# Optimization experiments

Hardware: AMD Instinct MI355X
Metric: run time of the kernel (lower is better)

The kernel has to match this reference:

```python
import jax, jax.numpy as jnp
import numpy as np

HID = 256   # hidden_dim
P = 16      # pool_size
EPS = 1e-5


def _ln(x, g, b):
    m = x.mean(-1, keepdims=True)
    v = x.var(-1, keepdims=True)
    return (x - m) * jax.lax.rsqrt(v + EPS) * g + b


def setup_inputs() -> dict:
    key = jax.random.key(0)
    ks = jax.random.split(key, 12)
    B, Cf, H, W = 8, 512, 64, 64
    Cg = Cf // 2
    Co = Cf // 2
    s = 0.02
    d = {}
    d['e_f'] = jax.random.normal(ks[0], (B, Cf, H, W), jnp.float32)
    d['e_g'] = jax.random.normal(ks[1], (B, Cg, H, W), jnp.float32)
    d['l_feat'] = jax.random.normal(ks[2], (B, 768, 20), jnp.float32)
    d['l_mask'] = jnp.ones((B, 20, 1), jnp.float32)
    d['ln_f_g'] = jnp.ones((Cf,), jnp.float32)
    d['ln_f_b'] = jnp.zeros((Cf,), jnp.float32)
    d['ln_g_g'] = jnp.ones((Cg,), jnp.float32)
    d['ln_g_b'] = jnp.zeros((Cg,), jnp.float32)
    d['wq'] = jax.random.normal(ks[3], (Cf, HID), jnp.float32) * s
    d['bq'] = jnp.zeros((HID,), jnp.float32)
    d['wk'] = jax.random.normal(ks[4], (Cg, HID), jnp.float32) * s
    d['bk'] = jnp.zeros((HID,), jnp.float32)
    d['wv'] = jax.random.normal(ks[5], (Cg, HID), jnp.float32) * s
    d['bv'] = jnp.zeros((HID,), jnp.float32)
    d['wo'] = jax.random.normal(ks[6], (HID, HID), jnp.float32) * s
    d['bo'] = jnp.zeros((HID,), jnp.float32)
    d['dw_k'] = jax.random.normal(ks[7], (HID, 1, 3, 3), jnp.float32) * s  # depthwise kernel (OIHW, I=1)
    d['efp_w'] = jax.random.normal(ks[8], (HID, Cf), jnp.float32) * s     # 1x1 conv v_channels->hidden
    d['efp_b'] = jnp.zeros((HID,), jnp.float32)
    d['outc_w'] = jax.random.normal(ks[9], (Co, HID), jnp.float32) * s    # 1x1 conv hidden->out
    d['outc_b'] = jnp.zeros((Co,), jnp.float32)
    d['bn_g'] = jnp.ones((Co,), jnp.float32)
    d['bn_b'] = jnp.zeros((Co,), jnp.float32)
    d['bn_m'] = jnp.zeros((Co,), jnp.float32)
    d['bn_v'] = jnp.ones((Co,), jnp.float32)
    return d


def reference(e_f, e_g, l_feat, l_mask, ln_f_g, ln_f_b, ln_g_g, ln_g_b,
              wq, bq, wk, bk, wv, bv, wo, bo, dw_k, efp_w, efp_b,
              outc_w, outc_b, bn_g, bn_b, bn_m, bn_v):
    B, Cf, H, W = e_f.shape
    # Q = w_qi(LN(e_f))                                  (B, HW, HID)
    q = _ln(e_f.transpose(0, 2, 3, 1), ln_f_g, ln_f_b).reshape(B, H * W, Cf) @ wq + bq
    # K/V projections from LN(e_g)
    g = _ln(e_g.transpose(0, 2, 3, 1), ln_g_g, ln_g_b).reshape(B, H * W, -1)
    k = (g @ wk + bk).reshape(B, H, W, HID)
    v = (g @ wv + bv).reshape(B, H, W, HID)
    # 16x16 max/avg pooling -> (B, Hp*Wp, HID)
    k = jnp.max(k.reshape(B, H // P, P, W // P, P, HID), axis=(2, 4)).reshape(B, -1, HID)
    v = jnp.mean(v.reshape(B, H // P, P, W // P, P, HID), axis=(2, 4)).reshape(B, -1, HID)
    # pooled attention
    attn = jax.nn.softmax(jnp.einsum('bqd,bkd->bqk', q, k) * (HID ** -0.5), axis=-1)
    a_i = jnp.einsum('bqk,bkd->bqd', attn, v)  # (B, HW, HID)
    # depthwise 3x3 conv on Q (NCHW)
    q_nchw = q.reshape(B, H, W, HID).transpose(0, 3, 1, 2)
    dw = jax.lax.conv_general_dilated(q_nchw, dw_k, (1, 1), [(1, 1), (1, 1)],
                                      feature_group_count=HID)
    combined = dw + a_i.reshape(B, H, W, HID).transpose(0, 3, 1, 2)
    comb = combined.transpose(0, 2, 3, 1).reshape(B, H * W, HID) @ wo + bo
    comb = comb.reshape(B, H, W, HID).transpose(0, 3, 1, 2)
    # 1x1 proj of e_f, elementwise gate
    efp = jnp.einsum('bchw,oc->bohw', e_f, efp_w) + efp_b[None, :, None, None]
    e_a = efp * comb
    # out: 1x1 conv + BN (inference) + ReLU (dropout inactive in eval)
    out = jnp.einsum('bchw,oc->bohw', e_a, outc_w) + outc_b[None, :, None, None]
    scale = (bn_g * jax.lax.rsqrt(bn_v + EPS))[None, :, None, None]
    out = (out - bn_m[None, :, None, None]) * scale + bn_b[None, :, None, None]
    return jax.nn.relu(out)
```

## Files before the change

### kernel.cpp

```cpp
#include <hip/hip_runtime.h>
#include <math.h>

#define EPS 1e-5f

typedef __attribute__((ext_vector_type(8))) short bf16x8;
typedef __attribute__((ext_vector_type(4))) float f32x4;

__device__ __forceinline__ unsigned short f2bf(float f) {
    unsigned int u = __float_as_uint(f);
    u += 0x7fff + ((u >> 16) & 1);
    return (unsigned short)(u >> 16);
}
__device__ __forceinline__ float bf2f(unsigned short h) {
    return __uint_as_float(((unsigned int)h) << 16);
}
__device__ __forceinline__ float lof(unsigned int u) {
    return __uint_as_float(u << 16);
}
__device__ __forceinline__ float hif(unsigned int u) {
    return __uint_as_float(u & 0xffff0000u);
}
__device__ __forceinline__ void async16(void* lds, const void* g) {
    __builtin_amdgcn_global_load_lds(
        (const __attribute__((address_space(1))) unsigned int*)g,
        (__attribute__((address_space(3))) unsigned int*)lds, 16, 0, 0);
}

__global__ __launch_bounds__(256) void prep_all(
    const float* __restrict__ lnfg, const float* __restrict__ lnfb,
    const float* __restrict__ wq, const float* __restrict__ bq,
    const float* __restrict__ efpw, const float* __restrict__ efpb,
    const float* __restrict__ lngg, const float* __restrict__ lngb,
    const float* __restrict__ wk, const float* __restrict__ bk,
    const float* __restrict__ wv, const float* __restrict__ bv,
    const float* __restrict__ wo, const float* __restrict__ outcw,
    const float* __restrict__ outcb, const float* __restrict__ bng,
    const float* __restrict__ bnb, const float* __restrict__ bnm,
    const float* __restrict__ bnv, const float* __restrict__ dwk,
    unsigned short* __restrict__ Wb1t, unsigned short* __restrict__ Wb2t,
    unsigned short* __restrict__ Wot, unsigned short* __restrict__ Woc,
    float* __restrict__ dwt,
    float* __restrict__ cs1, float* __restrict__ cst1,
    float* __restrict__ cs2, float* __restrict__ cst2,
    float* __restrict__ scv, float* __restrict__ shv)
{
    int idx = blockIdx.x * 256 + threadIdx.x;
    if (idx < 262144) {
        int n = idx >> 9, k = idx & 511;
        float v = (n < 256) ? lnfg[k] * wq[k * 256 + n]
                            : efpw[(size_t)(n - 256) * 512 + k];
        Wb1t[idx] = f2bf(v);
    } else if (idx < 327680) {
        int j = idx - 262144; int n = j >> 8, k = j & 255;
        Wb2t[j] = f2bf(lngg[k] * wk[k * 256 + n]);
    } else if (idx < 393216) {
        int j = idx - 327680; int n = j >> 8, k = j & 255;
        Wot[j] = f2bf(wo[k * 256 + n]);
    } else if (idx < 458752) {
        int j = idx - 393216;
        Woc[j] = f2bf(outcw[j]);
    } else if (idx < 461056) {
        int j = idx - 458752; int tap = j >> 8, ch = j & 255;
        dwt[j] = dwk[ch * 9 + tap];
    } else if (idx < 462336) {
        int j = idx - 461056;
        if (j < 256) {
            int n = j; float cs = 0.f, ct = 0.f;
            for (int k = 0; k < 512; k++) {
                float w = wq[k * 256 + n];
                cs += lnfg[k] * w; ct += lnfb[k] * w;
            }
            cs1[n] = cs; cst1[n] = ct + bq[n];
        } else if (j < 512) {
            cs1[j] = 0.f; cst1[j] = efpb[j - 256];
        } else if (j < 768) {
            int n = j - 512; float cs = 0.f, ct = 0.f;
            for (int k = 0; k < 256; k++) {
                float w = wk[k * 256 + n];
                cs += lngg[k] * w; ct += lngb[k] * w;
            }
            cs2[n] = cs; cst2[n] = ct + bk[n];
        } else if (j < 1024) {
            int n = j - 768; float cs = 0.f, ct = 0.f;
            for (int k = 0; k < 256; k++) {
                float w = wv[k * 256 + n];
                cs += lngg[k] * w; ct += lngb[k] * w;
            }
            cs2[256 + n] = cs; cst2[256 + n] = ct + bv[n];
        } else {
            int n = j - 1024;
            float s = bng[n] * rsqrtf(bnv[n] + EPS);
            scv[n] = s;
            shv[n] = (outcb[n] - bnm[n]) * s + bnb[n];
        }
    }
}

__global__ __launch_bounds__(256) void transpose_fg(
    const float* __restrict__ ef, const float* __restrict__ eg,
    unsigned short* __restrict__ ef_bf, unsigned short* __restrict__ eg_bf,
    float* __restrict__ pf, float* __restrict__ pfq,
    float* __restrict__ pg, float* __restrict__ pgq)
{
    __shared__ float tile[64][65];
    __shared__ float psum[4][64], pss[4][64];
    int id = blockIdx.x;
    const float* src; unsigned short* dst; float* ps; float* pq;
    int C, cblk, b, p0;
    if (id < 4096) {
        src = ef; dst = ef_bf; ps = pf; pq = pfq; C = 512;
        p0 = (id & 63) * 64; cblk = (id >> 6) & 7; b = id >> 9;
    } else {
        id -= 4096;
        src = eg; dst = eg_bf; ps = pg; pq = pgq; C = 256;
        p0 = (id & 63) * 64; cblk = (id >> 6) & 3; b = id >> 8;
    }
    int c0 = cblk * 64;
    const float* s = src + ((size_t)b * C + c0) * 4096 + p0;
    int t = threadIdx.x;
    int lane = t & 63, grp = t >> 6;
#pragma unroll
    for (int i = 0; i < 16; i++) {
        int c = i * 4 + grp;
        tile[c][lane] = s[(size_t)c * 4096 + lane];
    }
    __syncthreads();
    unsigned short* d = dst + ((size_t)(b * 4096 + p0)) * C + c0;
#pragma unroll
    for (int i = 0; i < 16; i++) {
        int p = i * 4 + grp;
        d[(size_t)p * C + lane] = f2bf(tile[lane][p]);
    }
    float sm = 0.f, sq = 0.f;
#pragma unroll
    for (int j = 0; j < 16; j++) {
        float v = tile[grp * 16 + j][lane];
        sm += v; sq += v * v;
    }
    psum[grp][lane] = sm; pss[grp][lane] = sq;
    __syncthreads();
    if (t < 64) {
        float fs = psum[0][t] + psum[1][t] + psum[2][t] + psum[3][t];
        float fq = pss[0][t] + pss[1][t] + pss[2][t] + pss[3][t];
        ps[cblk * 32768 + b * 4096 + p0 + t] = fs;
        pq[cblk * 32768 + b * 4096 + p0 + t] = fq;
    }
}

__global__ __launch_bounds__(256) void ln_finalize(
    const float* __restrict__ pf, const float* __restrict__ pfq,
    const float* __restrict__ pg, const float* __restrict__ pgq,
    float* __restrict__ mf, float* __restrict__ rf,
    float* __restrict__ mg, float* __restrict__ rg)
{
    int gp = blockIdx.x * 256 + threadIdx.x;
    float s = 0.f, q = 0.f;
#pragma unroll
    for (int i = 0; i < 8; i++) { s += pf[i * 32768 + gp]; q += pfq[i * 32768 + gp]; }
    float m = s * (1.f / 512.f);
    float v = q * (1.f / 512.f) - m * m;
    mf[gp] = m; rf[gp] = rsqrtf(v + EPS);
    s = 0.f; q = 0.f;
#pragma unroll
    for (int i = 0; i < 4; i++) { s += pg[i * 32768 + gp]; q += pgq[i * 32768 + gp]; }
    m = s * (1.f / 256.f);
    v = q * (1.f / 256.f) - m * m;
    mg[gp] = m; rg[gp] = rsqrtf(v + EPS);
}

template<int K>
__device__ __forceinline__ void mfma_core(
    const unsigned short* __restrict__ A, const unsigned short* __restrict__ Bt,
    int m0, int n0, unsigned short* As, unsigned short* Bs, f32x4 acc[4][4])
{
    const int tid = threadIdx.x;
    const int wave = tid >> 6, lane = tid & 63;
    const int wm = (wave & 1) * 64, wn = (wave >> 1) * 64;
#pragma unroll
    for (int i = 0; i < 4; i++)
#pragma unroll
        for (int j = 0; j < 4; j++) acc[i][j] = (f32x4){0.f, 0.f, 0.f, 0.f};

    const int srow = wave * 32 + (lane >> 3);
    const int sg = (lane & 7) ^ ((lane >> 3) & 7);
    const unsigned short* ga = A + (size_t)(m0 + srow) * K + sg * 8;
    const unsigned short* gb = Bt + (size_t)(n0 + srow) * K + sg * 8;

    for (int k0 = 0; k0 < K; k0 += 64) {
#pragma unroll
        for (int t = 0; t < 4; t++) {
            async16(As + (wave * 32 + t * 8) * 64, ga + (size_t)t * 8 * K + k0);
            async16(Bs + (wave * 32 + t * 8) * 64, gb + (size_t)t * 8 * K + k0);
        }
        __syncthreads();
#pragma unroll
        for (int ks = 0; ks < 2; ks++) {
            bf16x8 af[4], bfr[4];
            int kb = ks * 4 + (lane >> 4);
            int slot = (kb ^ (lane & 7)) * 8;
#pragma unroll
            for (int i = 0; i < 4; i++) {
                int m = wm + i * 16 + (lane & 15);
                af[i] = *(const bf16x8*)&As[m * 64 + slot];
                int n = wn + i * 16 + (lane & 15);
                bfr[i] = *(const bf16x8*)&Bs[n * 64 + slot];
            }
#pragma unroll
            for (int i = 0; i < 4; i++)
#pragma unroll
                for (int j = 0; j < 4; j++)
                    acc[i][j] = __builtin_amdgcn_mfma_f32_16x16x32_bf16(
                        af[i], bfr[j], acc[i][j], 0, 0, 0);
        }
        __syncthreads();
    }
}

__global__ __launch_bounds__(256) void gemm1_mfma(
    const unsigned short* __restrict__ ef_bf, const unsigned short* __restrict__ Wb1t,
    const float* __restrict__ cs1, const float* __restrict__ cst1,
    const float* __restrict__ mf, const float* __restrict__ rf,
    unsigned short* __restrict__ qbuf, unsigned short* __restrict__ efpbuf)
{
    __shared__ unsigned short As[8192], Bs[8192];
    f32x4 acc[4][4];
    int m0 = blockIdx.x * 128, n0 = blockIdx.y * 128;
    mfma_core<512>(ef_bf, Wb1t, m0, n0, As, Bs, acc);
    int lane = threadIdx.x & 63, wave = threadIdx.x >> 6;
    int wm = (wave & 1) * 64, wn = (wave >> 1) * 64;
    bool isq = (n0 < 256);
#pragma unroll
    for (int i = 0; i < 4; i++) {
#pragma unroll
        for (int r = 0; r < 4; r++) {
            int gm = m0 + wm + i * 16 + ((lane >> 4) * 4) + r;
            float mean = mf[gm], rs = rf[gm];
#pragma unroll
            for (int j = 0; j < 4; j++) {
                int n = n0 + wn + j * 16 + (lane & 15);
                float v = acc[i][j][r];
                if (isq) {
                    float o = rs * (v - mean * cs1[n]) + cst1[n];
                    qbuf[(size_t)gm * 256 + n] = f2bf(o);
                } else {
                    efpbuf[(size_t)gm * 256 + (n - 256)] = f2bf(v + cst1[n]);
                }
            }
        }
    }
}

__global__ __launch_bounds__(256) void gemm2k_mfma(
    const unsigned short* __restrict__ eg_bf, const unsigned short* __restrict__ Wb2t,
    const float* __restrict__ cs2, const float* __restrict__ cst2,
    const float* __restrict__ mg, const float* __restrict__ rg,
    unsigned short* __restrict__ kfull)
{
    __shared__ unsigned short As[8192], Bs[8192];
    f32x4 acc[4][4];
    int m0 = blockIdx.x * 128, n0 = blockIdx.y * 128;
    mfma_core<256>(eg_bf, Wb2t, m0, n0, As, Bs, acc);
    int lane = threadIdx.x & 63, wave = threadIdx.x >> 6;
    int wm = (wave & 1) * 64, wn = (wave >> 1) * 64;
#pragma unroll
    for (int i = 0; i < 4; i++) {
#pragma unroll
        for (int r = 0; r < 4; r++) {
            int gm = m0 + wm + i * 16 + ((lane >> 4) * 4) + r;
            float mean = mg[gm], rs = rg[gm];
#pragma unroll
            for (int j = 0; j < 4; j++) {
                int n = n0 + wn + j * 16 + (lane & 15);
                float o = rs * (acc[i][j][r] - mean * cs2[n]) + cst2[n];
                kfull[(size_t)gm * 256 + n] = f2bf(o);
            }
        }
    }
}

__global__ __launch_bounds__(256) void gemm3_mfma(
    const unsigned short* __restrict__ comb, const unsigned short* __restrict__ Wot,
    const float* __restrict__ bo, const unsigned short* __restrict__ efp,
    unsigned short* __restrict__ ea)
{
    __shared__ unsigned short As[8192], Bs[8192];
    f32x4 acc[4][4];
    int m0 = blockIdx.x * 128, n0 = blockIdx.y * 128;
    mfma_core<256>(comb, Wot, m0, n0, As, Bs, acc);
    int lane = threadIdx.x & 63, wave = threadIdx.x >> 6;
    int wm = (wave & 1) * 64, wn = (wave >> 1) * 64;
#pragma unroll
    for (int i = 0; i < 4; i++) {
#pragma unroll
        for (int r = 0; r < 4; r++) {
            int gm = m0 + wm + i * 16 + ((lane >> 4) * 4) + r;
#pragma unroll
            for (int j = 0; j < 4; j++) {
                int n = n0 + wn + j * 16 + (lane & 15);
                float o = (acc[i][j][r] + bo[n]) * bf2f(efp[(size_t)gm * 256 + n]);
                ea[(size_t)gm * 256 + n] = f2bf(o);
            }
        }
    }
}

__global__ __launch_bounds__(256) void gemm4_mfma(
    const unsigned short* __restrict__ Woc, const unsigned short* __restrict__ ea,
    const float* __restrict__ scv, const float* __restrict__ shv,
    float* __restrict__ outp)
{
    __shared__ unsigned short As[8192], Bs[8192];
    f32x4 acc[4][4];
    int m0 = blockIdx.x * 128, n0 = blockIdx.y * 128;
    mfma_core<256>(Woc, ea, m0, n0, As, Bs, acc);
    int lane = threadIdx.x & 63, wave = threadIdx.x >> 6;
    int wm = (wave & 1) * 64, wn = (wave >> 1) * 64;
#pragma unroll
    for (int i = 0; i < 4; i++) {
#pragma unroll
        for (int r = 0; r < 4; r++) {
            int co = m0 + wm + i * 16 + ((lane >> 4) * 4) + r;
            float s = scv[co], hh = shv[co];
#pragma unroll
            for (int j = 0; j < 4; j++) {
                int p = n0 + wn + j * 16 + (lane & 15);
                float o = fmaxf(fmaf(acc[i][j][r], s, hh), 0.f);
                outp[((size_t)(p >> 12)) * 1048576 + (size_t)co * 4096 + (p & 4095)] = o;
            }
        }
    }
}

__global__ __launch_bounds__(256) void pool_phase(
    const unsigned short* __restrict__ kfull, const float* __restrict__ eg,
    const float* __restrict__ rg, const float* __restrict__ mg,
    unsigned short* __restrict__ kpb, float* __restrict__ s1,
    float* __restrict__ s0)
{
    __shared__ float smem[4352];
    int id = blockIdx.x;
    int t = threadIdx.x;
    if (id < 128) {
        int b = id >> 4, cell = id & 15;
        int hp = cell >> 2, wp = cell & 3;
        int g8 = t & 31, rr = t >> 5;
        float kmx[8];
#pragma unroll
        for (int j = 0; j < 8; j++) kmx[j] = -3.402823466e38f;
#pragma unroll
        for (int rsub = 0; rsub < 2; rsub++) {
            int r = rr * 2 + rsub;
            int prow = (hp * 16 + r) * 64 + wp * 16;
            for (int cl = 0; cl < 16; cl++) {
                size_t basei = ((size_t)(b * 4096 + prow + cl)) * 256 + g8 * 8;
                uint4 kv = *(const uint4*)(kfull + basei);
                kmx[0] = fmaxf(kmx[0], lof(kv.x)); kmx[1] = fmaxf(kmx[1], hif(kv.x));
                kmx[2] = fmaxf(kmx[2], lof(kv.y)); kmx[3] = fmaxf(kmx[3], hif(kv.y));
                kmx[4] = fmaxf(kmx[4], lof(kv.z)); kmx[5] = fmaxf(kmx[5], hif(kv.z));
                kmx[6] = fmaxf(kmx[6], lof(kv.w)); kmx[7] = fmaxf(kmx[7], hif(kv.w));
            }
        }
#pragma unroll
        for (int j = 0; j < 8; j++) smem[rr * 256 + g8 * 8 + j] = kmx[j];
        __syncthreads();
        float m = smem[t];
#pragma unroll
        for (int r2 = 1; r2 < 8; r2++) m = fmaxf(m, smem[r2 * 256 + t]);
        kpb[(size_t)(b * 16 + cell) * 256 + t] = f2bf(m);
    } else {
        int id2 = id - 128;
        int b = id2 >> 6, hp = (id2 >> 4) & 3, cgrp = id2 & 15;
        int rr = t >> 4, cq = t & 15, cx = cq >> 2;
        int p = (hp * 16 + rr) * 64 + cq * 4;
        float4 w4 = *(const float4*)&rg[b * 4096 + p];
        float part[16];
        const float* egb = eg + ((size_t)b * 256 + cgrp * 16) * 4096 + p;
#pragma unroll
        for (int cc = 0; cc < 16; cc++) {
            float4 v4 = *(const float4*)(egb + (size_t)cc * 4096);
            part[cc] = w4.x * v4.x + w4.y * v4.y + w4.z * v4.z + w4.w * v4.w;
        }
#pragma unroll
        for (int cc = 0; cc < 16; cc++) smem[t * 16 + cc] = part[cc];
        if (cgrp == 0) {
            float4 m4 = *(const float4*)&mg[b * 4096 + p];
            smem[4096 + t] = w4.x * m4.x + w4.y * m4.y + w4.z * m4.z + w4.w * m4.w;
        }
        __syncthreads();
        if (t < 64) {
            int cx2 = t >> 4, cc = t & 15;
            float sacc = 0.f;
#pragma unroll
            for (int rr2 = 0; rr2 < 16; rr2++)
#pragma unroll
                for (int dq = 0; dq < 4; dq++)
                    sacc += smem[(rr2 * 16 + cx2 * 4 + dq) * 16 + cc];
            s1[((size_t)(b * 16 + hp * 4 + cx2)) * 256 + cgrp * 16 + cc] = sacc;
        }
        if (cgrp == 0 && t < 4) {
            float sacc = 0.f;
#pragma unroll
            for (int rr2 = 0; rr2 < 16; rr2++)
#pragma unroll
                for (int dq = 0; dq < 4; dq++)
                    sacc += smem[4096 + rr2 * 16 + t * 4 + dq];
            s0[b * 16 + hp * 4 + t] = sacc;
        }
    }
}

__global__ __launch_bounds__(256) void vpool_gemm(
    const float* __restrict__ s1, const float* __restrict__ s0,
    const float* __restrict__ lngg, const float* __restrict__ wv,
    const float* __restrict__ cs2, const float* __restrict__ cst2,
    float* __restrict__ vp)
{
    int cell = blockIdx.x;
    int n = threadIdx.x;
    const float* s1r = s1 + (size_t)cell * 256;
    float acc = 0.f;
    for (int c = 0; c < 256; c++)
        acc = fmaf(lngg[c] * s1r[c], wv[c * 256 + n], acc);
    vp[(size_t)cell * 256 + n] = acc * (1.f / 256.f)
        - (s0[cell] * (1.f / 256.f)) * cs2[256 + n] + cst2[256 + n];
}

__global__ __launch_bounds__(256) void combined_dw(
    const unsigned short* __restrict__ qbuf, const unsigned short* __restrict__ kpb,
    const float* __restrict__ vp, const float* __restrict__ dwt,
    unsigned short* __restrict__ combined)
{
    __shared__ float attns[256];
    int wave = threadIdx.x >> 6, lane = threadIdx.x & 63;
    int id = blockIdx.x;
    int b = id & 7, seg = id >> 3;
    int pidx0 = seg * 16;

    if (wave == 0) {
        int fr = lane & 15, quad = lane >> 4;
        const unsigned short* qrow = qbuf + (size_t)(b * 4096 + pidx0 + fr) * 256 + quad * 8;
        const unsigned short* krow = kpb + (size_t)(b * 16 + fr) * 256 + quad * 8;
        f32x4 sacc = {0.f, 0.f, 0.f, 0.f};
#pragma unroll
        for (int ks = 0; ks < 8; ks++) {
            bf16x8 af = *(const bf16x8*)(qrow + ks * 32);
            bf16x8 bf_ = *(const bf16x8*)(krow + ks * 32);
            sacc = __builtin_amdgcn_mfma_f32_16x16x32_bf16(af, bf_, sacc, 0, 0, 0);
        }
#pragma unroll
        for (int r = 0; r < 4; r++) {
            float s = sacc[r] * 0.0625f;
            float mx = s;
#pragma unroll
            for (int off = 8; off >= 1; off >>= 1) mx = fmaxf(mx, __shfl_xor(mx, off));
            float e = __expf(s - mx);
            float sum = e;
#pragma unroll
            for (int off = 8; off >= 1; off >>= 1) sum += __shfl_xor(sum, off);
            attns[(quad * 4 + r) * 16 + fr] = e / sum;
        }
    }
    __syncthreads();

    int pidx = pidx0 + wave * 4;
    int h = pidx >> 6, w0 = pidx & 63;
    int o4 = lane * 4;

    float4 kreg[9];
#pragma unroll
    for (int tap = 0; tap < 9; tap++)
        kreg[tap] = *(const float4*)&dwt[tap * 256 + o4];

    float4 acc[4];
#pragma unroll
    for (int i = 0; i < 4; i++) acc[i] = (float4){0.f, 0.f, 0.f, 0.f};

    const float* arow = attns + (wave * 4) * 16;
#pragma unroll
    for (int c = 0; c < 16; c++) {
        float4 v = *(const float4*)&vp[(size_t)(b * 16 + c) * 256 + o4];
#pragma unroll
        for (int i = 0; i < 4; i++) {
            float a = arow[i * 16 + c];
            acc[i].x = fmaf(a, v.x, acc[i].x); acc[i].y = fmaf(a, v.y, acc[i].y);
            acc[i].z = fmaf(a, v.z, acc[i].z); acc[i].w = fmaf(a, v.w, acc[i].w);
        }
    }
#pragma unroll
    for (int dy = 0; dy < 3; dy++) {
        int hh = h + dy - 1;
        if (hh < 0 || hh > 63) continue;
        const unsigned short* qr = qbuf + ((size_t)(b * 4096 + hh * 64)) * 256;
        float4 ft[6];
#pragma unroll
        for (int c = 0; c < 6; c++) {
            int xx = w0 - 1 + c;
            if (xx < 0 || xx > 63) {
                ft[c] = (float4){0.f, 0.f, 0.f, 0.f};
            } else {
                uint2 qa = *(const uint2*)(qr + (size_t)xx * 256 + o4);
                ft[c] = (float4){lof(qa.x), hif(qa.x), lof(qa.y), hif(qa.y)};
            }
        }
#pragma unroll
        for (int dx = 0; dx < 3; dx++) {
            float4 kk = kreg[dy * 3 + dx];
#pragma unroll
            for (int i = 0; i < 4; i++) {
                float4 qv = ft[i + dx];
                acc[i].x = fmaf(qv.x, kk.x, acc[i].x);
                acc[i].y = fmaf(qv.y, kk.y, acc[i].y);
                acc[i].z = fmaf(qv.z, kk.z, acc[i].z);
                acc[i].w = fmaf(qv.w, kk.w, acc[i].w);
            }
        }
    }
#pragma unroll
    for (int i = 0; i < 4; i++) {
        uint2 pk;
        pk.x = (unsigned)f2bf(acc[i].x) | ((unsigned)f2bf(acc[i].y) << 16);
        pk.y = (unsigned)f2bf(acc[i].z) | ((unsigned)f2bf(acc[i].w) << 16);
        *(uint2*)(combined + ((size_t)(b * 4096 + pidx + i)) * 256 + o4) = pk;
    }
}

extern "C" void kernel_launch(void* const* d_in, const int* in_sizes, int n_in,
                              void* d_out, int out_size, void* d_ws, size_t ws_size,
                              hipStream_t stream)
{
    const float* e_f   = (const float*)d_in[0];
    const float* e_g   = (const float*)d_in[1];
    const float* lnfg  = (const float*)d_in[4];
    const float* lnfb  = (const float*)d_in[5];
    const float* lngg  = (const float*)d_in[6];
    const float* lngb  = (const float*)d_in[7];
    const float* wq    = (const float*)d_in[8];
    const float* bq    = (const float*)d_in[9];
    const float* wk    = (const float*)d_in[10];
    const float* bk    = (const float*)d_in[11];
    const float* wv    = (const float*)d_in[12];
    const float* bv    = (const float*)d_in[13];
    const float* wo    = (const float*)d_in[14];
    const float* bo    = (const float*)d_in[15];
    const float* dwk   = (const float*)d_in[16];
    const float* efpw  = (const float*)d_in[17];
    const float* efpb  = (const float*)d_in[18];
    const float* outcw = (const float*)d_in[19];
    const float* outcb = (const float*)d_in[20];
    const float* bng   = (const float*)d_in[21];
    const float* bnb   = (const float*)d_in[22];
    const float* bnm   = (const float*)d_in[23];
    const float* bnv   = (const float*)d_in[24];
    float* outp = (float*)d_out;

    char* base = (char*)d_ws;
    auto alloc = [&](size_t bytes) -> char* {
        char* r = base; base += (bytes + 255) & ~(size_t)255; return r;
    };
    float* pf    = (float*)alloc(8 * 32768 * 4);
    float* pfq   = (float*)alloc(8 * 32768 * 4);
    float* pg    = (float*)alloc(4 * 32768 * 4);
    float* pgq   = (float*)alloc(4 * 32768 * 4);
    float* mf    = (float*)alloc(32768 * 4);
    float* rf    = (float*)alloc(32768 * 4);
    float* mg    = (float*)alloc(32768 * 4);
    float* rg    = (float*)alloc(32768 * 4);
    float* cs1   = (float*)alloc(512 * 4);
    float* cst1  = (float*)alloc(512 * 4);
    float* cs2   = (float*)alloc(512 * 4);
    float* cst2  = (float*)alloc(512 * 4);
    float* scv   = (float*)alloc(256 * 4);
    float* shv   = (float*)alloc(256 * 4);
    float* dwt   = (float*)alloc(9 * 256 * 4);
    unsigned short* Wb1t = (unsigned short*)alloc(262144 * 2);
    unsigned short* Wb2t = (unsigned short*)alloc(65536 * 2);
    unsigned short* Wot  = (unsigned short*)alloc(65536 * 2);
    unsigned short* Woc  = (unsigned short*)alloc(65536 * 2);
    unsigned short* ef_bf = (unsigned short*)alloc((size_t)32768 * 512 * 2);
    unsigned short* eg_bf = (unsigned short*)alloc((size_t)32768 * 256 * 2);
    unsigned short* qbuf  = (unsigned short*)alloc((size_t)32768 * 256 * 2);
    unsigned short* efpbuf = (unsigned short*)alloc((size_t)32768 * 256 * 2);
    unsigned short* kfull = (unsigned short*)alloc((size_t)32768 * 256 * 2);
    unsigned short* ea    = (unsigned short*)alloc((size_t)32768 * 256 * 2);
    unsigned short* kpb  = (unsigned short*)alloc(128 * 256 * 2);
    float* vp    = (float*)alloc(128 * 256 * 4);
    float* s1    = (float*)alloc(128 * 256 * 4);
    float* s0    = (float*)alloc(128 * 4);

    prep_all<<<1806, 256, 0, stream>>>(
        lnfg, lnfb, wq, bq, efpw, efpb, lngg, lngb, wk, bk, wv, bv, wo,
        outcw, outcb, bng, bnb, bnm, bnv, dwk,
        Wb1t, Wb2t, Wot, Woc, dwt, cs1, cst1, cs2, cst2, scv, shv);
    transpose_fg<<<6144, 256, 0, stream>>>(e_f, e_g, ef_bf, eg_bf,
                                           pf, pfq, pg, pgq);
    ln_finalize<<<128, 256, 0, stream>>>(pf, pfq, pg, pgq, mf, rf, mg, rg);
    gemm1_mfma<<<dim3(256, 4), 256, 0, stream>>>(ef_bf, Wb1t, cs1, cst1, mf, rf,
                                                 qbuf, efpbuf);
    gemm2k_mfma<<<dim3(256, 2), 256, 0, stream>>>(eg_bf, Wb2t, cs2, cst2, mg, rg,
                                                  kfull);
    pool_phase<<<640, 256, 0, stream>>>(kfull, e_g, rg, mg, kpb, s1, s0);
    vpool_gemm<<<128, 256, 0, stream>>>(s1, s0, lngg, wv, cs2, cst2, vp);
    combined_dw<<<2048, 256, 0, stream>>>(qbuf, kpb, vp, dwt, kfull);
    gemm3_mfma<<<dim3(256, 2), 256, 0, stream>>>(kfull, Wot, bo,
                                                 efpbuf, ea);
    gemm4_mfma<<<dim3(2, 256), 256, 0, stream>>>(Woc, ea, scv, shv, outp);
}
```

Measured before the change: 340.0 us.

## Fuse output projection and final 1x1 conv; pool V from bf16 e_g

```diff
diff --git a/kernel.cpp b/kernel.cpp
--- a/kernel.cpp
+++ b/kernel.cpp
@@ -278,66 +278,107 @@
     }
 }
 
-__global__ __launch_bounds__(256) void gemm3_mfma(
+__global__ __launch_bounds__(256) void gemm34_mfma(
     const unsigned short* __restrict__ comb, const unsigned short* __restrict__ Wot,
     const float* __restrict__ bo, const unsigned short* __restrict__ efp,
-    unsigned short* __restrict__ ea)
-{
-    __shared__ unsigned short As[8192], Bs[8192];
-    f32x4 acc[4][4];
-    int m0 = blockIdx.x * 128, n0 = blockIdx.y * 128;
-    mfma_core<256>(comb, Wot, m0, n0, As, Bs, acc);
-    int lane = threadIdx.x & 63, wave = threadIdx.x >> 6;
-    int wm = (wave & 1) * 64, wn = (wave >> 1) * 64;
-#pragma unroll
-    for (int i = 0; i < 4; i++) {
-#pragma unroll
-        for (int r = 0; r < 4; r++) {
-            int gm = m0 + wm + i * 16 + ((lane >> 4) * 4) + r;
-#pragma unroll
-            for (int j = 0; j < 4; j++) {
-                int n = n0 + wn + j * 16 + (lane & 15);
-                float o = (acc[i][j][r] + bo[n]) * bf2f(efp[(size_t)gm * 256 + n]);
-                ea[(size_t)gm * 256 + n] = f2bf(o);
-            }
-        }
-    }
-}
-
-__global__ __launch_bounds__(256) void gemm4_mfma(
-    const unsigned short* __restrict__ Woc, const unsigned short* __restrict__ ea,
+    const unsigned short* __restrict__ Woc,
     const float* __restrict__ scv, const float* __restrict__ shv,
     float* __restrict__ outp)
 {
-    __shared__ unsigned short As[8192], Bs[8192];
+    __shared__ unsigned short ea[64 * 256];
+    int wave = threadIdx.x >> 6, lane = threadIdx.x & 63;
+    int fr = lane & 15, quad = lane >> 4;
+    int m0 = blockIdx.x * 64;
+
     f32x4 acc[4][4];
-    int m0 = blockIdx.x * 128, n0 = blockIdx.y * 128;
-    mfma_core<256>(Woc, ea, m0, n0, As, Bs, acc);
-    int lane = threadIdx.x & 63, wave = threadIdx.x >> 6;
-    int wm = (wave & 1) * 64, wn = (wave >> 1) * 64;
+#pragma unroll
+    for (int i = 0; i < 4; i++)
+#pragma unroll
+        for (int j = 0; j < 4; j++) acc[i][j] = (f32x4){0.f, 0.f, 0.f, 0.f};
+#pragma unroll
+    for (int ks = 0; ks < 8; ks++) {
+        bf16x8 af[4], bfr[4];
+#pragma unroll
+        for (int i = 0; i < 4; i++)
+            af[i] = *(const bf16x8*)(comb +
+                     (size_t)(m0 + i * 16 + fr) * 256 + ks * 32 + quad * 8);
+#pragma unroll
+        for (int j = 0; j < 4; j++)
+            bfr[j] = *(const bf16x8*)(Wot +
+                     (size_t)(wave * 64 + j * 16 + fr) * 256 + ks * 32 + quad * 8);
+#pragma unroll
+        for (int i = 0; i < 4; i++)
+#pragma unroll
+            for (int j = 0; j < 4; j++)
+                acc[i][j] = __builtin_amdgcn_mfma_f32_16x16x32_bf16(
+                    af[i], bfr[j], acc[i][j], 0, 0, 0);
+    }
+#pragma unroll
+    for (int j = 0; j < 4; j++) {
+        int oc = wave * 64 + j * 16 + fr;
+        float bb = bo[oc];
+        int g = oc >> 3, sub = oc & 7;
+#pragma unroll
+        for (int i = 0; i < 4; i++) {
+#pragma unroll
+            for (int r = 0; r < 4; r++) {
+                int pl = i * 16 + quad * 4 + r;
+                float o = (acc[i][j][r] + bb) * bf2f(efp[(size_t)(m0 + pl) * 256 + oc]);
+                ea[pl * 256 + ((g ^ (pl & 7)) << 3) + sub] = f2bf(o);
+            }
+        }
+    }
+    __syncthreads();
+
+    f32x4 acc2[4][4];
+#pragma unroll
+    for (int i = 0; i < 4; i++)
+#pragma unroll
+        for (int j = 0; j < 4; j++) acc2[i][j] = (f32x4){0.f, 0.f, 0.f, 0.f};
+#pragma unroll
+    for (int ks = 0; ks < 8; ks++) {
+        bf16x8 af[4], bfr[4];
+#pragma unroll
+        for (int i = 0; i < 4; i++)
+            af[i] = *(const bf16x8*)(Woc +
+                     (size_t)(wave * 64 + i * 16 + fr) * 256 + ks * 32 + quad * 8);
+        int g = ks * 4 + quad;
+#pragma unroll
+        for (int j = 0; j < 4; j++) {
+            int pos = j * 16 + fr;
+            bfr[j] = *(const bf16x8*)&ea[pos * 256 + ((g ^ (fr & 7)) << 3)];
+        }
+#pragma unroll
+        for (int i = 0; i < 4; i++)
+#pragma unroll
+            for (int j = 0; j < 4; j++)
+                acc2[i][j] = __builtin_amdgcn_mfma_f32_16x16x32_bf16(
+                    af[i], bfr[j], acc2[i][j], 0, 0, 0);
+    }
+    int b_ = m0 >> 12, p0 = m0 & 4095;
 #pragma unroll
     for (int i = 0; i < 4; i++) {
 #pragma unroll
         for (int r = 0; r < 4; r++) {
-            int co = m0 + wm + i * 16 + ((lane >> 4) * 4) + r;
+            int co = wave * 64 + i * 16 + quad * 4 + r;
             float s = scv[co], hh = shv[co];
 #pragma unroll
             for (int j = 0; j < 4; j++) {
-                int p = n0 + wn + j * 16 + (lane & 15);
-                float o = fmaxf(fmaf(acc[i][j][r], s, hh), 0.f);
-                outp[((size_t)(p >> 12)) * 1048576 + (size_t)co * 4096 + (p & 4095)] = o;
+                int p = p0 + j * 16 + fr;
+                float o = fmaxf(fmaf(acc2[i][j][r], s, hh), 0.f);
+                outp[(size_t)b_ * 1048576 + (size_t)co * 4096 + p] = o;
             }
         }
     }
 }
 
 __global__ __launch_bounds__(256) void pool_phase(
-    const unsigned short* __restrict__ kfull, const float* __restrict__ eg,
+    const unsigned short* __restrict__ kfull, const unsigned short* __restrict__ eg_bf,
     const float* __restrict__ rg, const float* __restrict__ mg,
     unsigned short* __restrict__ kpb, float* __restrict__ s1,
     float* __restrict__ s0)
 {
-    __shared__ float smem[4352];
+    __shared__ float smem[2048];
     int id = blockIdx.x;
     int t = threadIdx.x;
     if (id < 128) {
@@ -369,42 +410,26 @@
         kpb[(size_t)(b * 16 + cell) * 256 + t] = f2bf(m);
     } else {
         int id2 = id - 128;
-        int b = id2 >> 6, hp = (id2 >> 4) & 3, cgrp = id2 & 15;
-        int rr = t >> 4, cq = t & 15, cx = cq >> 2;
-        int p = (hp * 16 + rr) * 64 + cq * 4;
-        float4 w4 = *(const float4*)&rg[b * 4096 + p];
-        float part[16];
-        const float* egb = eg + ((size_t)b * 256 + cgrp * 16) * 4096 + p;
-#pragma unroll
-        for (int cc = 0; cc < 16; cc++) {
-            float4 v4 = *(const float4*)(egb + (size_t)cc * 4096);
-            part[cc] = w4.x * v4.x + w4.y * v4.y + w4.z * v4.z + w4.w * v4.w;
-        }
-#pragma unroll
-        for (int cc = 0; cc < 16; cc++) smem[t * 16 + cc] = part[cc];
-        if (cgrp == 0) {
-            float4 m4 = *(const float4*)&mg[b * 4096 + p];
-            smem[4096 + t] = w4.x * m4.x + w4.y * m4.y + w4.z * m4.z + w4.w * m4.w;
-        }
+        int b = id2 >> 4, cell = id2 & 15;
+        int hp = cell >> 2, wp = cell & 3;
+        int pt = b * 4096 + (hp * 16 + (t >> 4)) * 64 + wp * 16 + (t & 15);
+        smem[t] = rg[pt] * mg[pt];
+        float accv = 0.f;
+        for (int r = 0; r < 16; r++) {
+            int prow = b * 4096 + (hp * 16 + r) * 64 + wp * 16;
+#pragma unroll 4
+            for (int c2 = 0; c2 < 16; c2++) {
+                int p = prow + c2;
+                accv = fmaf(rg[p], bf2f(eg_bf[(size_t)p * 256 + t]), accv);
+            }
+        }
+        s1[(size_t)id2 * 256 + t] = accv;
         __syncthreads();
         if (t < 64) {
-            int cx2 = t >> 4, cc = t & 15;
-            float sacc = 0.f;
-#pragma unroll
-            for (int rr2 = 0; rr2 < 16; rr2++)
-#pragma unroll
-                for (int dq = 0; dq < 4; dq++)
-                    sacc += smem[(rr2 * 16 + cx2 * 4 + dq) * 16 + cc];
-            s1[((size_t)(b * 16 + hp * 4 + cx2)) * 256 + cgrp * 16 + cc] = sacc;
-        }
-        if (cgrp == 0 && t < 4) {
-            float sacc = 0.f;
-#pragma unroll
-            for (int rr2 = 0; rr2 < 16; rr2++)
-#pragma unroll
-                for (int dq = 0; dq < 4; dq++)
-                    sacc += smem[4096 + rr2 * 16 + t * 4 + dq];
-            s0[b * 16 + hp * 4 + t] = sacc;
+            float v = smem[t] + smem[t + 64] + smem[t + 128] + smem[t + 192];
+#pragma unroll
+            for (int off = 32; off >= 1; off >>= 1) v += __shfl_down(v, off);
+            if (t == 0) s0[id2] = v;
         }
     }
 }
@@ -581,7 +606,6 @@
     unsigned short* qbuf  = (unsigned short*)alloc((size_t)32768 * 256 * 2);
     unsigned short* efpbuf = (unsigned short*)alloc((size_t)32768 * 256 * 2);
     unsigned short* kfull = (unsigned short*)alloc((size_t)32768 * 256 * 2);
-    unsigned short* ea    = (unsigned short*)alloc((size_t)32768 * 256 * 2);
     unsigned short* kpb  = (unsigned short*)alloc(128 * 256 * 2);
     float* vp    = (float*)alloc(128 * 256 * 4);
     float* s1    = (float*)alloc(128 * 256 * 4);
@@ -598,10 +622,9 @@
                                                  qbuf, efpbuf);
     gemm2k_mfma<<<dim3(256, 2), 256, 0, stream>>>(eg_bf, Wb2t, cs2, cst2, mg, rg,
                                                   kfull);
-    pool_phase<<<640, 256, 0, stream>>>(kfull, e_g, rg, mg, kpb, s1, s0);
+    pool_phase<<<256, 256, 0, stream>>>(kfull, eg_bf, rg, mg, kpb, s1, s0);
     vpool_gemm<<<128, 256, 0, stream>>>(s1, s0, lngg, wv, cs2, cst2, vp);
     combined_dw<<<2048, 256, 0, stream>>>(qbuf, kpb, vp, dwt, kfull);
-    gemm3_mfma<<<dim3(256, 2), 256, 0, stream>>>(kfull, Wot, bo,
-                                                 efpbuf, ea);
-    gemm4_mfma<<<dim3(2, 256), 256, 0, stream>>>(Woc, ea, scv, shv, outp);
-}
+    gemm34_mfma<<<512, 256, 0, stream>>>(kfull, Wot, bo, efpbuf,
+                                         Woc, scv, shv, outp);
+}
```

After: 353.9 us. 1.04x slower.
